# Kernel optimization log

Measured on AMD Instinct MI355X. Metric: run time of the kernel, lower is better.

## Reference

```python
import jax, jax.numpy as jnp
import numpy as np

B = 65536
IN_F = 512
OUT_F = 256
NUM_GROUPS = 8
EPS = 1e-5


def setup_inputs() -> dict:
    key = jax.random.key(0)
    ks = jax.random.split(key, 6)
    return {
        "x": jax.random.normal(ks[0], (B, IN_F), dtype=jnp.float32),
        "weight": jax.random.normal(ks[1], (OUT_F, IN_F), dtype=jnp.float32) * 0.05,
        "bias_linear": jax.random.normal(ks[2], (OUT_F,), dtype=jnp.float32) * 0.05,
        "weight_gn": jax.random.normal(ks[3], (OUT_F,), dtype=jnp.float32),
        "bias_gn": jax.random.normal(ks[4], (OUT_F,), dtype=jnp.float32),
        "bias": jax.random.normal(ks[5], (1, OUT_F, 1, 1), dtype=jnp.float32),
    }


def reference(x, weight, bias_linear, weight_gn, bias_gn, bias):
    # Linear: (B, IN_F) @ (IN_F, OUT_F) + bias -> (B, OUT_F)
    h = jnp.einsum("bi,oi->bo", x, weight) + bias_linear
    # GroupNorm over channel dim (dim=1) with NUM_GROUPS groups
    g = h.reshape(B, NUM_GROUPS, OUT_F // NUM_GROUPS)
    mean = jnp.mean(g, axis=2, keepdims=True)
    var = jnp.mean(jnp.square(g - mean), axis=2, keepdims=True)
    gn = ((g - mean) * jax.lax.rsqrt(var + EPS)).reshape(B, OUT_F)
    gn = gn * weight_gn + bias_gn
    # Min over channels, keepdim -> (B, 1)
    min_vals = jnp.min(gn, axis=1, keepdims=True)
    # torch broadcasting: (B,1) + (1,256,1,1) -> (1,256,B,1)
    result = min_vals + bias
    return result
```

## Files before the change

### kernel.cpp

```cpp
#include <hip/hip_runtime.h>
#include <hip/hip_bf16.h>

#define B_ROWS 65536
#define K_DIM  512
#define N_DIM  256
#define EPS    1e-5f
#define MTILE  32
#define NBLK   256
#define TPB    8
#define ROWS_PER_BLK (MTILE * TPB)
#define STRIDE 520

using short8  = __attribute__((ext_vector_type(8))) short;
using floatx4 = __attribute__((ext_vector_type(4))) float;

#define LBAR() do {                                          \
    __builtin_amdgcn_sched_barrier(0);                       \
    asm volatile("s_waitcnt lgkmcnt(0)" ::: "memory");       \
    __builtin_amdgcn_s_barrier();                            \
    __builtin_amdgcn_sched_barrier(0);                       \
} while (0)

__device__ __forceinline__ unsigned short f2bf(float f) {
    unsigned u = __builtin_bit_cast(unsigned, f);
    u += 0x7FFFu + ((u >> 16) & 1u);
    return (unsigned short)(u >> 16);
}

__global__ __launch_bounds__(64) void pack_w(const float* __restrict__ W,
                                             unsigned short* __restrict__ P) {
    int b    = blockIdx.x;
    int nt   = b >> 4, kk = b & 15;
    int lane = threadIdx.x;
    int l15  = lane & 15, quad = lane >> 4;
    const float* src = W + (size_t)(nt * 16 + l15) * K_DIM + kk * 32 + quad * 8;
    short8 v;
#pragma unroll
    for (int j = 0; j < 8; ++j) v[j] = (short)f2bf(src[j]);
    *(short8*)(P + ((size_t)(nt * 16 + kk) * 64 + lane) * 8) = v;
}

__global__ __launch_bounds__(1024) void fused_persistent(
    const float* __restrict__ X, const unsigned short* __restrict__ P,
    const float* __restrict__ bias_lin, const float* __restrict__ wgn,
    const float* __restrict__ bgn, const float* __restrict__ bias,
    float* __restrict__ out)
{
    __shared__ unsigned short Ash[2][MTILE * STRIDE];
    __shared__ float smS[16][32];
    __shared__ float smSS[16][32];
    __shared__ float smin[16][32];
    __shared__ float m_sh[ROWS_PER_BLK];

    const int tid  = threadIdx.x;
    const int wave = tid >> 6;
    const int lane = tid & 63;
    const int l15  = lane & 15, quad = lane >> 4;

    short8 bfr[16];
#pragma unroll
    for (int kkg = 0; kkg < 16; ++kkg)
        bfr[kkg] = *(const short8*)(P + (((size_t)wave * 16 + kkg) * 64 + lane) * 8);

    float blr[4], wgr[4], bgr[4];
#pragma unroll
    for (int r = 0; r < 4; ++r) {
        int c = wave * 16 + quad * 4 + r;
        blr[r] = bias_lin[c]; wgr[r] = wgn[c]; bgr[r] = bgn[c];
    }
    const float bias_c = bias[tid >> 2];

    const int r0 = (tid >> 7) * 4;
    const int c4 = (tid & 127) * 4;

    const size_t row_base = (size_t)blockIdx.x * ROWS_PER_BLK;

    float4 xq[4];
#pragma unroll
    for (int p = 0; p < 4; ++p)
        xq[p] = *(const float4*)(X + (row_base + r0 + p) * K_DIM + c4);
#pragma unroll
    for (int p = 0; p < 4; ++p) {
        ushort4 h;
        h.x = f2bf(xq[p].x); h.y = f2bf(xq[p].y);
        h.z = f2bf(xq[p].z); h.w = f2bf(xq[p].w);
        *(ushort4*)(&Ash[0][(r0 + p) * STRIDE + c4]) = h;
    }
#pragma unroll
    for (int p = 0; p < 4; ++p)
        xq[p] = *(const float4*)(X + (row_base + MTILE + r0 + p) * K_DIM + c4);
    LBAR();

    int cur = 0;
    for (int it = 0; it < TPB; ++it) {
        if (it + 1 < TPB) {
#pragma unroll
            for (int p = 0; p < 4; ++p) {
                ushort4 h;
                h.x = f2bf(xq[p].x); h.y = f2bf(xq[p].y);
                h.z = f2bf(xq[p].z); h.w = f2bf(xq[p].w);
                *(ushort4*)(&Ash[cur ^ 1][(r0 + p) * STRIDE + c4]) = h;
            }
            if (it + 2 < TPB) {
#pragma unroll
                for (int p = 0; p < 4; ++p)
                    xq[p] = *(const float4*)(X + (row_base + (size_t)(it + 2) * MTILE + r0 + p) * K_DIM + c4);
            }
        }

        floatx4 acc[2];
#pragma unroll
        for (int rt = 0; rt < 2; ++rt)
#pragma unroll
            for (int r = 0; r < 4; ++r) acc[rt][r] = blr[r];
#pragma unroll
        for (int kk = 0; kk < 16; ++kk) {
            short8 a0 = *(const short8*)&Ash[cur][(l15)      * STRIDE + kk * 32 + quad * 8];
            short8 a1 = *(const short8*)&Ash[cur][(16 + l15) * STRIDE + kk * 32 + quad * 8];
            acc[0] = __builtin_amdgcn_mfma_f32_16x16x32_bf16(bfr[kk], a0, acc[0], 0, 0, 0);
            acc[1] = __builtin_amdgcn_mfma_f32_16x16x32_bf16(bfr[kk], a1, acc[1], 0, 0, 0);
        }

        float sreg[2], ssreg[2];
#pragma unroll
        for (int rt = 0; rt < 2; ++rt) {
            float s = 0.f, ss = 0.f;
#pragma unroll
            for (int r = 0; r < 4; ++r) { float v = acc[rt][r]; s += v; ss = fmaf(v, v, ss); }
            s  += __shfl_xor(s, 16);  s  += __shfl_xor(s, 32);
            ss += __shfl_xor(ss, 16); ss += __shfl_xor(ss, 32);
            sreg[rt] = s; ssreg[rt] = ss;
            if (quad == 0) { smS[wave][rt * 16 + l15] = s; smSS[wave][rt * 16 + l15] = ss; }
        }
        LBAR();

#pragma unroll
        for (int rt = 0; rt < 2; ++rt) {
            int row = rt * 16 + l15;
            float st   = sreg[rt]  + smS[wave ^ 1][row];
            float sst  = ssreg[rt] + smSS[wave ^ 1][row];
            float mean = st * (1.0f / 32.0f);
            float var  = sst * (1.0f / 32.0f) - mean * mean;
            float inv  = rsqrtf(var + EPS);
            float mi   = mean * inv;
            float mn   = 1e30f;
#pragma unroll
            for (int r = 0; r < 4; ++r) {
                float g = fmaf(fmaf(acc[rt][r], inv, -mi), wgr[r], bgr[r]);
                mn = fminf(mn, g);
            }
            mn = fminf(mn, __shfl_xor(mn, 16));
            mn = fminf(mn, __shfl_xor(mn, 32));
            if (quad == 0) smin[wave][row] = mn;
        }
        LBAR();

        if (tid < MTILE) {
            float m0 = smin[0][tid];
#pragma unroll
            for (int w = 1; w < 16; ++w) m0 = fminf(m0, smin[w][tid]);
            m_sh[it * MTILE + tid] = m0;
        }
        cur ^= 1;
    }

    LBAR();
    {
        int c = tid >> 2;
        int q = tid & 3;
        float* dst = out + (size_t)c * B_ROWS + row_base + q * 64;
#pragma unroll
        for (int i = 0; i < 16; ++i) {
            float4 mv = *(const float4*)&m_sh[q * 64 + i * 4];
            float4 o;
            o.x = mv.x + bias_c; o.y = mv.y + bias_c;
            o.z = mv.z + bias_c; o.w = mv.w + bias_c;
            *(float4*)(dst + i * 4) = o;
        }
    }
}

extern "C" void kernel_launch(void* const* d_in, const int* in_sizes, int n_in,
                              void* d_out, int out_size, void* d_ws, size_t ws_size,
                              hipStream_t stream) {
    const float* x    = (const float*)d_in[0];
    const float* w    = (const float*)d_in[1];
    const float* bl   = (const float*)d_in[2];
    const float* wg   = (const float*)d_in[3];
    const float* bg   = (const float*)d_in[4];
    const float* bias = (const float*)d_in[5];

    unsigned short* P = (unsigned short*)d_ws;
    float* out = (float*)d_out;

    hipLaunchKernelGGL(pack_w, dim3(256), dim3(64), 0, stream, w, P);
    hipLaunchKernelGGL(fused_persistent, dim3(NBLK), dim3(1024), 0, stream,
                       x, P, bl, wg, bg, bias, out);
}
```

Measured before the change: 239.5 us.

## Keep X rows stationary in registers and stream weights through shared memory

```diff
diff --git a/kernel.cpp b/kernel.cpp
--- a/kernel.cpp
+++ b/kernel.cpp
@@ -1,18 +1,15 @@
 #include <hip/hip_runtime.h>
-#include <hip/hip_bf16.h>
 
 #define B_ROWS 65536
 #define K_DIM  512
 #define N_DIM  256
 #define EPS    1e-5f
-#define MTILE  32
 #define NBLK   256
-#define TPB    8
-#define ROWS_PER_BLK (MTILE * TPB)
-#define STRIDE 520
+#define RPB    256
 
 using short8  = __attribute__((ext_vector_type(8))) short;
 using floatx4 = __attribute__((ext_vector_type(4))) float;
+using int4v   = __attribute__((ext_vector_type(4))) int;
 
 #define LBAR() do {                                          \
     __builtin_amdgcn_sched_barrier(0);                       \
@@ -40,141 +37,147 @@
     *(short8*)(P + ((size_t)(nt * 16 + kk) * 64 + lane) * 8) = v;
 }
 
-__global__ __launch_bounds__(1024) void fused_persistent(
+__global__ __launch_bounds__(512, 2) void fused_xstat(
     const float* __restrict__ X, const unsigned short* __restrict__ P,
     const float* __restrict__ bias_lin, const float* __restrict__ wgn,
     const float* __restrict__ bgn, const float* __restrict__ bias,
     float* __restrict__ out)
 {
-    __shared__ unsigned short Ash[2][MTILE * STRIDE];
-    __shared__ float smS[16][32];
-    __shared__ float smSS[16][32];
-    __shared__ float smin[16][32];
-    __shared__ float m_sh[ROWS_PER_BLK];
+    __shared__ unsigned short Wsh[8 * 16 * 64 * 8];
+    __shared__ float par_sh[3 * N_DIM];
+    __shared__ float m_sh[RPB];
 
     const int tid  = threadIdx.x;
     const int wave = tid >> 6;
     const int lane = tid & 63;
     const int l15  = lane & 15, quad = lane >> 4;
 
-    short8 bfr[16];
-#pragma unroll
-    for (int kkg = 0; kkg < 16; ++kkg)
-        bfr[kkg] = *(const short8*)(P + (((size_t)wave * 16 + kkg) * 64 + lane) * 8);
-
-    float blr[4], wgr[4], bgr[4];
-#pragma unroll
-    for (int r = 0; r < 4; ++r) {
-        int c = wave * 16 + quad * 4 + r;
-        blr[r] = bias_lin[c]; wgr[r] = wgn[c]; bgr[r] = bgn[c];
-    }
-    const float bias_c = bias[tid >> 2];
-
-    const int r0 = (tid >> 7) * 4;
-    const int c4 = (tid & 127) * 4;
-
-    const size_t row_base = (size_t)blockIdx.x * ROWS_PER_BLK;
-
-    float4 xq[4];
-#pragma unroll
-    for (int p = 0; p < 4; ++p)
-        xq[p] = *(const float4*)(X + (row_base + r0 + p) * K_DIM + c4);
-#pragma unroll
-    for (int p = 0; p < 4; ++p) {
-        ushort4 h;
-        h.x = f2bf(xq[p].x); h.y = f2bf(xq[p].y);
-        h.z = f2bf(xq[p].z); h.w = f2bf(xq[p].w);
-        *(ushort4*)(&Ash[0][(r0 + p) * STRIDE + c4]) = h;
-    }
-#pragma unroll
-    for (int p = 0; p < 4; ++p)
-        xq[p] = *(const float4*)(X + (row_base + MTILE + r0 + p) * K_DIM + c4);
+    const size_t row_base = (size_t)blockIdx.x * RPB;
+
+    if (tid < N_DIM) {
+        par_sh[tid]             = bias_lin[tid];
+        par_sh[N_DIM + tid]     = wgn[tid];
+        par_sh[2 * N_DIM + tid] = bgn[tid];
+    }
+
+    const int4v* Pv = (const int4v*)P;
+    int4v*       Wv = (int4v*)Wsh;
+#pragma unroll
+    for (int i = 0; i < 16; ++i)
+        Wv[i * 512 + tid] = Pv[i * 512 + tid];
+
+    short8 xf[2][16];
+#pragma unroll
+    for (int rt = 0; rt < 2; ++rt) {
+        const float* xrow = X + (row_base + wave * 32 + rt * 16 + l15) * K_DIM + quad * 8;
+#pragma unroll
+        for (int kkg = 0; kkg < 16; ++kkg) {
+            float4 lo = *(const float4*)(xrow + kkg * 32);
+            float4 hi = *(const float4*)(xrow + kkg * 32 + 4);
+            short8 v;
+            v[0] = (short)f2bf(lo.x); v[1] = (short)f2bf(lo.y);
+            v[2] = (short)f2bf(lo.z); v[3] = (short)f2bf(lo.w);
+            v[4] = (short)f2bf(hi.x); v[5] = (short)f2bf(hi.y);
+            v[6] = (short)f2bf(hi.z); v[7] = (short)f2bf(hi.w);
+            xf[rt][kkg] = v;
+        }
+    }
     LBAR();
 
-    int cur = 0;
-    for (int it = 0; it < TPB; ++it) {
-        if (it + 1 < TPB) {
-#pragma unroll
-            for (int p = 0; p < 4; ++p) {
-                ushort4 h;
-                h.x = f2bf(xq[p].x); h.y = f2bf(xq[p].y);
-                h.z = f2bf(xq[p].z); h.w = f2bf(xq[p].w);
-                *(ushort4*)(&Ash[cur ^ 1][(r0 + p) * STRIDE + c4]) = h;
+    float rmin[2] = { 1e30f, 1e30f };
+
+#pragma unroll
+    for (int h = 0; h < 2; ++h) {
+        if (h == 1) {
+            LBAR();
+#pragma unroll
+            for (int i = 0; i < 16; ++i)
+                Wv[i * 512 + tid] = Pv[8192 + i * 512 + tid];
+            LBAR();
+        }
+
+#pragma unroll
+        for (int g4 = 0; g4 < 4; ++g4) {
+            const int gbase = h * 128 + g4 * 32;
+            float bl_[2][4], wg_[2][4], bg_[2][4];
+#pragma unroll
+            for (int ntp = 0; ntp < 2; ++ntp)
+#pragma unroll
+                for (int r = 0; r < 4; ++r) {
+                    int ch = gbase + ntp * 16 + quad * 4 + r;
+                    bl_[ntp][r] = par_sh[ch];
+                    wg_[ntp][r] = par_sh[N_DIM + ch];
+                    bg_[ntp][r] = par_sh[2 * N_DIM + ch];
+                }
+
+            floatx4 acc[2][2];
+#pragma unroll
+            for (int ntp = 0; ntp < 2; ++ntp)
+#pragma unroll
+                for (int rt = 0; rt < 2; ++rt)
+#pragma unroll
+                    for (int r = 0; r < 4; ++r)
+                        acc[ntp][rt][r] = bl_[ntp][r];
+
+#pragma unroll
+            for (int ntp = 0; ntp < 2; ++ntp) {
+                const int ntl = g4 * 2 + ntp;
+#pragma unroll
+                for (int kkg = 0; kkg < 16; ++kkg) {
+                    short8 wv = *(const short8*)&Wsh[(((size_t)ntl * 16 + kkg) * 64 + lane) * 8];
+                    acc[ntp][0] = __builtin_amdgcn_mfma_f32_16x16x32_bf16(wv, xf[0][kkg], acc[ntp][0], 0, 0, 0);
+                    acc[ntp][1] = __builtin_amdgcn_mfma_f32_16x16x32_bf16(wv, xf[1][kkg], acc[ntp][1], 0, 0, 0);
+                }
             }
-            if (it + 2 < TPB) {
-#pragma unroll
-                for (int p = 0; p < 4; ++p)
-                    xq[p] = *(const float4*)(X + (row_base + (size_t)(it + 2) * MTILE + r0 + p) * K_DIM + c4);
+
+#pragma unroll
+            for (int rt = 0; rt < 2; ++rt) {
+                float s = 0.f, ss = 0.f;
+#pragma unroll
+                for (int ntp = 0; ntp < 2; ++ntp)
+#pragma unroll
+                    for (int r = 0; r < 4; ++r) {
+                        float v = acc[ntp][rt][r];
+                        s += v; ss = fmaf(v, v, ss);
+                    }
+                s  += __shfl_xor(s, 16);  s  += __shfl_xor(s, 32);
+                ss += __shfl_xor(ss, 16); ss += __shfl_xor(ss, 32);
+                float mean = s * (1.0f / 32.0f);
+                float var  = ss * (1.0f / 32.0f) - mean * mean;
+                float inv  = rsqrtf(var + EPS);
+                float mi   = mean * inv;
+                float mn   = rmin[rt];
+#pragma unroll
+                for (int ntp = 0; ntp < 2; ++ntp)
+#pragma unroll
+                    for (int r = 0; r < 4; ++r) {
+                        float g = fmaf(fmaf(acc[ntp][rt][r], inv, -mi), wg_[ntp][r], bg_[ntp][r]);
+                        mn = fminf(mn, g);
+                    }
+                rmin[rt] = mn;
             }
         }
-
-        floatx4 acc[2];
-#pragma unroll
-        for (int rt = 0; rt < 2; ++rt)
-#pragma unroll
-            for (int r = 0; r < 4; ++r) acc[rt][r] = blr[r];
-#pragma unroll
-        for (int kk = 0; kk < 16; ++kk) {
-            short8 a0 = *(const short8*)&Ash[cur][(l15)      * STRIDE + kk * 32 + quad * 8];
-            short8 a1 = *(const short8*)&Ash[cur][(16 + l15) * STRIDE + kk * 32 + quad * 8];
-            acc[0] = __builtin_amdgcn_mfma_f32_16x16x32_bf16(bfr[kk], a0, acc[0], 0, 0, 0);
-            acc[1] = __builtin_amdgcn_mfma_f32_16x16x32_bf16(bfr[kk], a1, acc[1], 0, 0, 0);
-        }
-
-        float sreg[2], ssreg[2];
-#pragma unroll
-        for (int rt = 0; rt < 2; ++rt) {
-            float s = 0.f, ss = 0.f;
-#pragma unroll
-            for (int r = 0; r < 4; ++r) { float v = acc[rt][r]; s += v; ss = fmaf(v, v, ss); }
-            s  += __shfl_xor(s, 16);  s  += __shfl_xor(s, 32);
-            ss += __shfl_xor(ss, 16); ss += __shfl_xor(ss, 32);
-            sreg[rt] = s; ssreg[rt] = ss;
-            if (quad == 0) { smS[wave][rt * 16 + l15] = s; smSS[wave][rt * 16 + l15] = ss; }
-        }
-        LBAR();
-
-#pragma unroll
-        for (int rt = 0; rt < 2; ++rt) {
-            int row = rt * 16 + l15;
-            float st   = sreg[rt]  + smS[wave ^ 1][row];
-            float sst  = ssreg[rt] + smSS[wave ^ 1][row];
-            float mean = st * (1.0f / 32.0f);
-            float var  = sst * (1.0f / 32.0f) - mean * mean;
-            float inv  = rsqrtf(var + EPS);
-            float mi   = mean * inv;
-            float mn   = 1e30f;
-#pragma unroll
-            for (int r = 0; r < 4; ++r) {
-                float g = fmaf(fmaf(acc[rt][r], inv, -mi), wgr[r], bgr[r]);
-                mn = fminf(mn, g);
-            }
-            mn = fminf(mn, __shfl_xor(mn, 16));
-            mn = fminf(mn, __shfl_xor(mn, 32));
-            if (quad == 0) smin[wave][row] = mn;
-        }
-        LBAR();
-
-        if (tid < MTILE) {
-            float m0 = smin[0][tid];
-#pragma unroll
-            for (int w = 1; w < 16; ++w) m0 = fminf(m0, smin[w][tid]);
-            m_sh[it * MTILE + tid] = m0;
-        }
-        cur ^= 1;
-    }
-
+    }
+
+#pragma unroll
+    for (int rt = 0; rt < 2; ++rt) {
+        float mn = rmin[rt];
+        mn = fminf(mn, __shfl_xor(mn, 16));
+        mn = fminf(mn, __shfl_xor(mn, 32));
+        if (quad == 0) m_sh[wave * 32 + rt * 16 + l15] = mn;
+    }
     LBAR();
+
     {
-        int c = tid >> 2;
-        int q = tid & 3;
-        float* dst = out + (size_t)c * B_ROWS + row_base + q * 64;
-#pragma unroll
-        for (int i = 0; i < 16; ++i) {
-            float4 mv = *(const float4*)&m_sh[q * 64 + i * 4];
+        int c = tid >> 1;
+        int q = tid & 1;
+        float bc = bias[c];
+        float* dst = out + (size_t)c * B_ROWS + row_base + q * 128;
+#pragma unroll
+        for (int i = 0; i < 32; ++i) {
+            float4 mv = *(const float4*)&m_sh[q * 128 + i * 4];
             float4 o;
-            o.x = mv.x + bias_c; o.y = mv.y + bias_c;
-            o.z = mv.z + bias_c; o.w = mv.w + bias_c;
+            o.x = mv.x + bc; o.y = mv.y + bc; o.z = mv.z + bc; o.w = mv.w + bc;
             *(float4*)(dst + i * 4) = o;
         }
     }
@@ -194,6 +197,6 @@
     float* out = (float*)d_out;
 
     hipLaunchKernelGGL(pack_w, dim3(256), dim3(64), 0, stream, w, P);
-    hipLaunchKernelGGL(fused_persistent, dim3(NBLK), dim3(1024), 0, stream,
+    hipLaunchKernelGGL(fused_xstat, dim3(NBLK), dim3(512), 0, stream,
                        x, P, bl, wg, bg, bias, out);
 }
```

Result: slower. 276.3 us (+15.4%).
